# Kernel tuning notes

Measured on AMD Instinct MI355X. Metric: run time of the kernel, lower is better.

Reference implementation:

```python
import jax, jax.numpy as jnp
import numpy as np
from jax import lax

# ---- config (mirrors cfg.* used by the module) ----
ANCHOR_RATIOS = (0.5, 1.0, 2.0)
ANCHOR_SCALES = (8.0, 16.0, 32.0)
FEATURE_STRIDE = 16
BASE_SIZE = 40  # generate_anchors(40, ...)
BN_EPS = 1e-5
LOG_CLAMP = 1e-30  # torch uses 1e-300, which underflows to 0 in fp32; use fp32-safe tiny


def generate_anchors(base_size=BASE_SIZE, ratios=ANCHOR_RATIOS, scales=ANCHOR_SCALES):
    """py-faster-rcnn style anchor generation, corner format (x1,y1,x2,y2). -> (A,4)"""
    w = h = float(base_size)
    cx = (base_size - 1) * 0.5
    cy = (base_size - 1) * 0.5
    size = w * h
    out = []
    for r in ratios:
        ws = np.round(np.sqrt(size / r))
        hs = np.round(ws * r)
        for s in scales:
            W, H = ws * s, hs * s
            out.append([cx - 0.5 * (W - 1), cy - 0.5 * (H - 1),
                        cx + 0.5 * (W - 1), cy + 0.5 * (H - 1)])
    return np.asarray(out, dtype=np.float32)  # (A,4)


def splash_anchors(fH, fW, n, base_anchors, stride):
    """Shift base anchors over the feature grid. -> (n, fH*fW*A, 4), row-major H,W then A."""
    sx = jnp.arange(fW, dtype=jnp.float32) * stride
    sy = jnp.arange(fH, dtype=jnp.float32) * stride
    SY, SX = jnp.meshgrid(sy, sx, indexing='ij')            # (fH,fW)
    shifts = jnp.stack([SX, SY, SX, SY], axis=-1).reshape(-1, 1, 4)  # (fH*fW,1,4)
    anc = (shifts + jnp.asarray(base_anchors)[None, :, :]).reshape(-1, 4)  # (fH*fW*A,4)
    return jnp.broadcast_to(anc[None], (n, anc.shape[0], 4))


def conv2d(x, w, b, pad):
    y = lax.conv_general_dilated(x, w, (1, 1), [(pad, pad), (pad, pad)],
                                 dimension_numbers=('NCHW', 'OIHW', 'NCHW'))
    return y + b[None, :, None, None]


def batchnorm_train(x, gamma, beta):
    # training-mode BN: per-channel batch stats over (N,H,W), biased variance
    m = jnp.mean(x, axis=(0, 2, 3), keepdims=True)
    v = jnp.mean(jnp.square(x - m), axis=(0, 2, 3), keepdims=True)
    xn = (x - m) * lax.rsqrt(v + BN_EPS)
    return xn * gamma[None, :, None, None] + beta[None, :, None, None]


def mish(x):
    return x * jnp.tanh(jax.nn.softplus(x))


def corner2center(b):
    w = b[..., 2] - b[..., 0]
    h = b[..., 3] - b[..., 1]
    cx = b[..., 0] + 0.5 * w
    cy = b[..., 1] + 0.5 * h
    return jnp.stack([cx, cy, w, h], axis=-1)


def setup_inputs() -> dict:
    key = jax.random.key(0)
    ks = jax.random.split(key, 7)
    C_IN, C_BASE, A = 256, 256, 9
    x = jax.random.normal(ks[0], (8, C_IN, 128, 128), dtype=jnp.float32)
    # kaiming-uniform-ish scaled weights
    def kaiming(k, shape):
        fan_in = shape[1] * shape[2] * shape[3]
        bound = float(np.sqrt(6.0 / fan_in))
        return jax.random.uniform(k, shape, jnp.float32, -bound, bound)
    return {
        "x": x,
        "W_base": kaiming(ks[1], (C_BASE, C_IN, 3, 3)),
        "b_base": jnp.zeros((C_BASE,), jnp.float32),
        "g_base": jnp.ones((C_BASE,), jnp.float32),
        "be_base": jnp.zeros((C_BASE,), jnp.float32),
        "W_cls": kaiming(ks[2], (2 * A, C_BASE, 1, 1)),
        "b_cls": jnp.zeros((2 * A,), jnp.float32),
        "g_cls": jnp.ones((2 * A,), jnp.float32),
        "be_cls": jnp.zeros((2 * A,), jnp.float32),
        "W_reg": kaiming(ks[3], (4 * A, C_BASE, 1, 1)),
        "b_reg": jnp.zeros((4 * A,), jnp.float32),
        "g_reg": jnp.ones((4 * A,), jnp.float32),
        "be_reg": jnp.zeros((4 * A,), jnp.float32),
        "img_size": 2048,
    }


def reference(x, W_base, b_base, g_base, be_base,
              W_cls, b_cls, g_cls, be_cls,
              W_reg, b_reg, g_reg, be_reg, img_size):
    n, c, fH, fW = x.shape
    A = 9
    # BASE_CONV: Conv3x3 -> Mish -> Dropout2d (identity here, deterministic) -> BN
    base = batchnorm_train(mish(conv2d(x, W_base, b_base, 1)), g_base, be_base)

    anchors = splash_anchors(fH, fW, n, generate_anchors(), FEATURE_STRIDE)  # (n,K,4) corners

    rpn_reg = batchnorm_train(conv2d(base, W_reg, b_reg, 0), g_reg, be_reg)
    rpn_reg = jnp.transpose(rpn_reg, (0, 2, 3, 1)).reshape(n, -1, 4)          # (n,K,4)

    rpn_score = batchnorm_train(conv2d(base, W_cls, b_cls, 0), g_cls, be_cls)
    rpn_score = jnp.transpose(rpn_score, (0, 2, 3, 1)).reshape(n, fH, fW, A, 2)
    fg_scores = jax.nn.softmax(rpn_score, axis=4)[..., 1].reshape(n, -1)      # (n,K)

    rpn_reg = rpn_reg + anchors                                               # decoded corners

    # proposal layer: clip proposals to the image, keep all (fixed-shape)
    lim = jnp.float32(img_size)
    rois = jnp.clip(rpn_reg, 0.0, lim)                                        # (n,K,4) corners
    rois = corner2center(rois)                                                # (cx,cy,w,h)

    anc_c = corner2center(anchors)
    tx = (rois[..., 0] - anc_c[..., 0]) / anc_c[..., 2]
    ty = (rois[..., 1] - anc_c[..., 1]) / anc_c[..., 3]
    tw = jnp.log(jnp.maximum(rois[..., 2] / anc_c[..., 2], LOG_CLAMP))
    th = jnp.log(jnp.maximum(rois[..., 3] / anc_c[..., 3], LOG_CLAMP))
    ts = jnp.stack([tx, ty, tw, th], axis=-1)
    return (fg_scores, ts, rois)
```

## Files before the change

### kernel.cpp

```cpp
#include <hip/hip_runtime.h>
#include <stdint.h>

typedef short bf16x8 __attribute__((ext_vector_type(8)));
typedef float f32x4 __attribute__((ext_vector_type(4)));

#define AS1 __attribute__((address_space(1)))
#define AS3 __attribute__((address_space(3)))

static __device__ __forceinline__ void gl16(const void* g, void* l) {
  __builtin_amdgcn_global_load_lds((const AS1 void*)g, (AS3 void*)l, 16, 0, 0);
}

static __device__ __forceinline__ unsigned short f2bf(float f) {
  unsigned u = __float_as_uint(f);
  u = u + 0x7fffu + ((u >> 16) & 1u);
  return (unsigned short)(u >> 16);
}
static __device__ __forceinline__ float bf2f(unsigned short h) {
  return __uint_as_float(((unsigned)h) << 16);
}
static __device__ __forceinline__ float mishf(float x) {
  float sp = fmaxf(x, 0.f) + log1pf(expf(-fabsf(x)));
  float e2 = expf(-2.f * sp);
  float th = (1.f - e2) / (1.f + e2);
  return x * th;
}

#define NIMG 8
#define HH 128
#define WW 128
#define HP 130
#define CIN 256
#define MPIX (NIMG * HH * WW)
#define KTOT 2304
#define FGCNT (MPIX * 9)
#define TSCNT (MPIX * 9 * 4)

__device__ __constant__ float AW[9] = {456.f, 912.f, 1824.f, 320.f, 640.f, 1280.f, 224.f, 448.f, 896.f};
__device__ __constant__ float AH[9] = {224.f, 448.f, 896.f, 320.f, 640.f, 1280.f, 448.f, 896.f, 1792.f};

__global__ __launch_bounds__(256) void k_wt(const float* __restrict__ Wb,
                                            unsigned short* __restrict__ Wt2) {
  int d = blockIdx.x * 256 + threadIdx.x;
  int c = d & 31, oc = (d >> 5) & 255, s = d >> 13;
  int kh = s / 24, r = s % 24, kw = r >> 3, icb = r & 7;
  int ic = icb * 32 + c;
  Wt2[d] = f2bf(Wb[((oc * 256 + ic) * 3 + kh) * 3 + kw]);
}

__global__ __launch_bounds__(256) void k_tr(const float* __restrict__ x,
                                            unsigned short* __restrict__ xt2) {
  __shared__ float tile[32][129];
  int b = blockIdx.x;
  int icb = b & 7, h = (b >> 3) & 127, n = b >> 10;
  int t = threadIdx.x;
  const float* src = x + (((size_t)(n * 256 + icb * 32) * 128 + h) * 128);
#pragma unroll
  for (int i = 0; i < 4; ++i) {
    int idx = t + 256 * i;
    int w4 = idx & 31, ic = idx >> 5;
    float4 v = *(const float4*)(src + (size_t)ic * 16384 + w4 * 4);
    tile[ic][w4 * 4 + 0] = v.x; tile[ic][w4 * 4 + 1] = v.y;
    tile[ic][w4 * 4 + 2] = v.z; tile[ic][w4 * 4 + 3] = v.w;
  }
  __syncthreads();
#pragma unroll
  for (int i = 0; i < 8; ++i) {
    int idx = t + 256 * i;
    int icp = idx & 15, w = idx >> 4;
    unsigned lo = f2bf(tile[icp * 2][w]);
    unsigned hi = f2bf(tile[icp * 2 + 1][w]);
    size_t pix = ((size_t)(icb * 8 + n) * HP + (h + 1)) * HP + (w + 1);
    *(unsigned*)(xt2 + pix * 32 + icp * 2) = lo | (hi << 16);
  }
}

__global__ __launch_bounds__(256) void k_bord(unsigned short* __restrict__ xt2) {
  int tid = blockIdx.x * 256 + threadIdx.x;
  int chunk = tid & 3, pix = tid >> 2;
  int nn = pix / 516, bp = pix % 516;
  int hp, wp;
  if (bp < 130) { hp = 0; wp = bp; }
  else if (bp < 260) { hp = 129; wp = bp - 130; }
  else { int r = bp - 260; hp = 1 + (r >> 1); wp = (r & 1) ? 129 : 0; }
  size_t off = (((size_t)nn * HP + hp) * HP + wp) * 32 + chunk * 8;
  uint4 z = {0u, 0u, 0u, 0u};
  *(uint4*)(xt2 + off) = z;
}

__global__ __launch_bounds__(256) void k_conv(const unsigned short* __restrict__ xt2,
                                              const unsigned short* __restrict__ Wt2,
                                              const float* __restrict__ b_base,
                                              unsigned short* __restrict__ yt2,
                                              float* __restrict__ statsA) {
  __shared__ __align__(16) char lds[16384];
  int t = threadIdx.x;
  int lane = t & 63, w4 = t >> 6;
  int wr = w4 >> 1, wc = w4 & 1;
  int row16 = lane & 15, kgl = lane >> 4;
  int pr = lane & 15, pq = lane >> 4;

  int bid = blockIdx.x;
  int swz = (bid & 7) * 256 + (bid >> 3);
  int pixb = swz >> 1, oh = swz & 1;
  int n = pixb >> 7, h0 = pixb & 127;
  size_t M0 = (size_t)pixb * 128;

  f32x4 acc[4][4];
#pragma unroll
  for (int m = 0; m < 4; ++m)
#pragma unroll
    for (int nf = 0; nf < 4; ++nf) { f32x4 z = {0.f, 0.f, 0.f, 0.f}; acc[m][nf] = z; }

  const unsigned short* aS0 =
      xt2 + ((size_t)(n * HP + h0) * HP + w4 * 32 + pr) * 32 + pq * 8;
  const unsigned short* aS1 = aS0 + 16 * 32;
  const unsigned short* bS0 = Wt2 + (size_t)(oh * 128 + w4 * 32 + pr) * 32 + pq * 8;
  const unsigned short* bS1 = bS0 + 16 * 32;
  char* dA0 = lds + (2 * w4) * 1024;
  char* dA1 = lds + (2 * w4 + 1) * 1024;
  char* dB0 = lds + 8192 + (2 * w4) * 1024;
  char* dB1 = lds + 8192 + (2 * w4 + 1) * 1024;

  int aoffA = wr * 4096 + kgl * 256 + row16 * 16;
  int aoffB = wc * 4096 + kgl * 256 + row16 * 16;
  const size_t planeStride = (size_t)8 * HP * HP * 32;

  int s = 0;
  for (int kh = 0; kh < 3; ++kh) {
    for (int kw = 0; kw < 3; ++kw) {
      for (int icb = 0; icb < 8; ++icb, ++s) {
        size_t offA = (size_t)icb * planeStride + ((size_t)kh * HP + kw) * 32;
        size_t offB = (size_t)s * 8192;
        gl16(aS0 + offA, dA0);
        gl16(aS1 + offA, dA1);
        gl16(bS0 + offB, dB0);
        gl16(bS1 + offB, dB1);
        __syncthreads();
        bf16x8 af[4], bfr[4];
#pragma unroll
        for (int m = 0; m < 4; ++m) af[m] = *(const bf16x8*)(lds + aoffA + m * 1024);
#pragma unroll
        for (int nf = 0; nf < 4; ++nf) bfr[nf] = *(const bf16x8*)(lds + 8192 + aoffB + nf * 1024);
#pragma unroll
        for (int m = 0; m < 4; ++m)
#pragma unroll
          for (int nf = 0; nf < 4; ++nf)
            acc[m][nf] = __builtin_amdgcn_mfma_f32_16x16x32_bf16(af[m], bfr[nf], acc[m][nf], 0, 0, 0);
        __syncthreads();
      }
    }
  }

  float sums[4] = {0.f, 0.f, 0.f, 0.f}, sumq[4] = {0.f, 0.f, 0.f, 0.f};
#pragma unroll
  for (int nf = 0; nf < 4; ++nf) {
    int oc = oh * 128 + wc * 64 + nf * 16 + row16;
    float bias = b_base[oc];
    size_t obase = (size_t)(oc >> 5) * MPIX * 32 + (oc & 31);
#pragma unroll
    for (int m = 0; m < 4; ++m) {
#pragma unroll
      for (int j = 0; j < 4; ++j) {
        int p = wr * 64 + m * 16 + kgl * 4 + j;
        float y = mishf(acc[m][nf][j] + bias);
        yt2[obase + (M0 + p) * 32] = f2bf(y);
        sums[nf] += y; sumq[nf] += y * y;
      }
    }
  }
#pragma unroll
  for (int nf = 0; nf < 4; ++nf) {
    float s1 = sums[nf], s2 = sumq[nf];
    s1 += __shfl_xor(s1, 16); s2 += __shfl_xor(s2, 16);
    s1 += __shfl_xor(s1, 32); s2 += __shfl_xor(s2, 32);
    if (lane < 16) {
      int oc = oh * 128 + wc * 64 + nf * 16 + lane;
      atomicAdd(&statsA[oc], s1);
      atomicAdd(&statsA[256 + oc], s2);
    }
  }
}

__global__ __launch_bounds__(256) void k_fold(const float* __restrict__ statsA,
                                              const float* __restrict__ g_base,
                                              const float* __restrict__ be_base,
                                              const float* __restrict__ W_cls,
                                              const float* __restrict__ b_cls,
                                              const float* __restrict__ W_reg,
                                              const float* __restrict__ b_reg,
                                              unsigned short* __restrict__ W2t2,
                                              float* __restrict__ b2) {
  __shared__ float sS[256], sT[256];
  int t = threadIdx.x;
  {
    float cnt = (float)MPIX;
    float m = statsA[t] / cnt;
    float v = fmaxf(statsA[256 + t] / cnt - m * m, 0.f);
    float s = g_base[t] * rsqrtf(v + 1e-5f);
    sS[t] = s;
    sT[t] = be_base[t] - m * s;
  }
  __syncthreads();
  if (t < 64) {
    float bias = 0.f;
    if (t < 36) bias = b_reg[t];
    else if (t < 54) bias = b_cls[t - 36];
    float acc = 0.f;
    for (int ic = 0; ic < 256; ++ic) {
      float w = 0.f;
      if (t < 36) w = W_reg[t * 256 + ic];
      else if (t < 54) w = W_cls[(t - 36) * 256 + ic];
      acc += w * sT[ic];
      W2t2[((size_t)(ic >> 5) * 64 + t) * 32 + (ic & 31)] = f2bf(w * sS[ic]);
    }
    b2[t] = bias + acc;
  }
}

__global__ __launch_bounds__(256) void k_mm2(const unsigned short* __restrict__ yt2,
                                             const unsigned short* __restrict__ W2t2,
                                             const float* __restrict__ b2,
                                             unsigned short* __restrict__ zt,
                                             float* __restrict__ statsZ) {
  __shared__ __align__(16) char lds2[12288];
  int t = threadIdx.x, lane = t & 63, w4 = t >> 6;
  int row16 = lane & 15, kgl = lane >> 4;
  int pr = lane & 15, pq = lane >> 4;
  size_t pixbase = (size_t)blockIdx.x * 128;

  f32x4 acc[2][4];
#pragma unroll
  for (int m = 0; m < 2; ++m)
#pragma unroll
    for (int nn = 0; nn < 4; ++nn) { f32x4 z = {0.f, 0.f, 0.f, 0.f}; acc[m][nn] = z; }

  const unsigned short* aS0 = yt2 + (pixbase + w4 * 32 + pr) * 32 + pq * 8;
  const unsigned short* aS1 = aS0 + 16 * 32;
  const unsigned short* bS = W2t2 + (size_t)(w4 * 16 + pr) * 32 + pq * 8;
  char* dA0 = lds2 + (2 * w4) * 1024;
  char* dA1 = lds2 + (2 * w4 + 1) * 1024;
  char* dB  = lds2 + 8192 + w4 * 1024;

  int aoffA = w4 * 2048 + kgl * 256 + row16 * 16;
  int aoffB = kgl * 256 + row16 * 16;

  for (int s = 0; s < 8; ++s) {
    size_t ao = (size_t)s * MPIX * 32;
    size_t bo = (size_t)s * 2048;
    gl16(aS0 + ao, dA0);
    gl16(aS1 + ao, dA1);
    gl16(bS + bo, dB);
    __syncthreads();
    bf16x8 af[2], bfr[4];
#pragma unroll
    for (int m = 0; m < 2; ++m) af[m] = *(const bf16x8*)(lds2 + aoffA + m * 1024);
#pragma unroll
    for (int nn = 0; nn < 4; ++nn) bfr[nn] = *(const bf16x8*)(lds2 + 8192 + aoffB + nn * 1024);
#pragma unroll
    for (int m = 0; m < 2; ++m)
#pragma unroll
      for (int nn = 0; nn < 4; ++nn)
        acc[m][nn] = __builtin_amdgcn_mfma_f32_16x16x32_bf16(af[m], bfr[nn], acc[m][nn], 0, 0, 0);
    __syncthreads();
  }

  float sums[4] = {0.f, 0.f, 0.f, 0.f}, sumq[4] = {0.f, 0.f, 0.f, 0.f};
#pragma unroll
  for (int nn = 0; nn < 4; ++nn) {
    int oc = nn * 16 + row16;
    float bias = b2[oc];
#pragma unroll
    for (int m = 0; m < 2; ++m) {
#pragma unroll
      for (int j = 0; j < 4; ++j) {
        int p = w4 * 32 + m * 16 + kgl * 4 + j;
        float v = acc[m][nn][j] + bias;
        zt[(pixbase + p) * 64 + oc] = f2bf(v);
        sums[nn] += v; sumq[nn] += v * v;
      }
    }
  }
#pragma unroll
  for (int nn = 0; nn < 4; ++nn) {
    float s1 = sums[nn], s2 = sumq[nn];
    s1 += __shfl_xor(s1, 16); s2 += __shfl_xor(s2, 16);
    s1 += __shfl_xor(s1, 32); s2 += __shfl_xor(s2, 32);
    if (lane < 16) {
      int oc = nn * 16 + lane;
      atomicAdd(&statsZ[oc], s1);
      atomicAdd(&statsZ[64 + oc], s2);
    }
  }
}

__global__ __launch_bounds__(64) void k_zstat(const float* __restrict__ statsZ,
                                              const float* __restrict__ g_cls,
                                              const float* __restrict__ be_cls,
                                              const float* __restrict__ g_reg,
                                              const float* __restrict__ be_reg,
                                              float* __restrict__ zsc,
                                              float* __restrict__ zsh) {
  int t = threadIdx.x;
  float g = 1.f, be = 0.f;
  if (t < 36) { g = g_reg[t]; be = be_reg[t]; }
  else if (t < 54) { g = g_cls[t - 36]; be = be_cls[t - 36]; }
  float cnt = (float)MPIX;
  float m = statsZ[t] / cnt;
  float v = fmaxf(statsZ[64 + t] / cnt - m * m, 0.f);
  float s = g * rsqrtf(v + 1e-5f);
  zsc[t] = s;
  zsh[t] = be - m * s;
}

__global__ __launch_bounds__(256) void k_dec(const unsigned short* __restrict__ zt,
                                             const float* __restrict__ zsc,
                                             const float* __restrict__ zsh,
                                             const int* __restrict__ imgsz,
                                             float* __restrict__ out) {
  int p = blockIdx.x * 256 + threadIdx.x;
  float lim = (float)imgsz[0];
  float zn[64];
  {
    const uint4* zp4 = (const uint4*)(zt + (size_t)p * 64);
#pragma unroll
    for (int i = 0; i < 8; ++i) {
      uint4 v = zp4[i];
      unsigned a0 = v.x, a1 = v.y, a2 = v.z, a3 = v.w;
      zn[i * 8 + 0] = bf2f((unsigned short)(a0 & 0xffff));
      zn[i * 8 + 1] = bf2f((unsigned short)(a0 >> 16));
      zn[i * 8 + 2] = bf2f((unsigned short)(a1 & 0xffff));
      zn[i * 8 + 3] = bf2f((unsigned short)(a1 >> 16));
      zn[i * 8 + 4] = bf2f((unsigned short)(a2 & 0xffff));
      zn[i * 8 + 5] = bf2f((unsigned short)(a2 >> 16));
      zn[i * 8 + 6] = bf2f((unsigned short)(a3 & 0xffff));
      zn[i * 8 + 7] = bf2f((unsigned short)(a3 >> 16));
    }
#pragma unroll
    for (int i = 0; i < 54; ++i) zn[i] = zn[i] * zsc[i] + zsh[i];
  }
  int rem = p & 16383, h = rem >> 7, w = rem & 127;
  float fx = 16.f * (float)w, fy = 16.f * (float)h;
  size_t kbase = (size_t)p * 9;
  float* fgout = out;
  float* tsout = out + FGCNT;
  float* roout = out + FGCNT + TSCNT;
#pragma unroll
  for (int a = 0; a < 9; ++a) {
    float x1 = 20.f - 0.5f * AW[a] + fx;
    float y1 = 20.f - 0.5f * AH[a] + fy;
    float x2 = 19.f + 0.5f * AW[a] + fx;
    float y2 = 19.f + 0.5f * AH[a] + fy;
    float cx1 = fminf(fmaxf(x1 + zn[4 * a + 0], 0.f), lim);
    float cy1 = fminf(fmaxf(y1 + zn[4 * a + 1], 0.f), lim);
    float cx2 = fminf(fmaxf(x2 + zn[4 * a + 2], 0.f), lim);
    float cy2 = fminf(fmaxf(y2 + zn[4 * a + 3], 0.f), lim);
    float bw = cx2 - cx1, bh = cy2 - cy1;
    float cx = cx1 + 0.5f * bw, cy = cy1 + 0.5f * bh;
    float aw = AW[a] - 1.f, ah = AH[a] - 1.f;
    float acx = 19.5f + fx, acy = 19.5f + fy;
    float tx = (cx - acx) / aw, ty = (cy - acy) / ah;
    float tw = logf(fmaxf(bw / aw, 1e-30f));
    float th = logf(fmaxf(bh / ah, 1e-30f));
    float s0 = zn[36 + 2 * a], s1 = zn[36 + 2 * a + 1];
    float fg = 1.f / (1.f + expf(s0 - s1));
    fgout[kbase + a] = fg;
    size_t o4 = (kbase + a) * 4;
    tsout[o4 + 0] = tx; tsout[o4 + 1] = ty; tsout[o4 + 2] = tw; tsout[o4 + 3] = th;
    roout[o4 + 0] = cx; roout[o4 + 1] = cy; roout[o4 + 2] = bw; roout[o4 + 3] = bh;
  }
}

extern "C" void kernel_launch(void* const* d_in, const int* in_sizes, int n_in,
                              void* d_out, int out_size, void* d_ws, size_t ws_size,
                              hipStream_t stream) {
  const float* x   = (const float*)d_in[0];
  const float* Wb  = (const float*)d_in[1];
  const float* bb  = (const float*)d_in[2];
  const float* gb  = (const float*)d_in[3];
  const float* beb = (const float*)d_in[4];
  const float* Wc  = (const float*)d_in[5];
  const float* bc  = (const float*)d_in[6];
  const float* gc  = (const float*)d_in[7];
  const float* bec = (const float*)d_in[8];
  const float* Wr  = (const float*)d_in[9];
  const float* br  = (const float*)d_in[10];
  const float* gr  = (const float*)d_in[11];
  const float* ber = (const float*)d_in[12];
  const int* imgsz = (const int*)d_in[13];

  char* ws = (char*)d_ws;
  const size_t OFF_XTP = 0;
  const size_t OFF_Y   = 69222400;
  const size_t OFF_Z   = 136331264;
  const size_t OFF_WT  = 153108480;
  const size_t OFF_W2  = 154288128;
  const size_t OFF_S   = 154320896;
  unsigned short* xt2  = (unsigned short*)(ws + OFF_XTP);
  unsigned short* yt2  = (unsigned short*)(ws + OFF_Y);
  unsigned short* zt   = (unsigned short*)(ws + OFF_Z);
  unsigned short* Wt2  = (unsigned short*)(ws + OFF_WT);
  unsigned short* W2t2 = (unsigned short*)(ws + OFF_W2);
  float* b2     = (float*)(ws + OFF_S);
  float* statsA = (float*)(ws + OFF_S + 256);
  float* statsZ = (float*)(ws + OFF_S + 2304);
  float* zsc    = (float*)(ws + OFF_S + 2816);
  float* zsh    = (float*)(ws + OFF_S + 3072);
  float* out = (float*)d_out;

  hipMemsetAsync(statsA, 0, (512 + 128) * sizeof(float), stream);
  k_wt  <<<2304, 256, 0, stream>>>(Wb, Wt2);
  k_tr  <<<8192, 256, 0, stream>>>(x, xt2);
  k_bord<<<516, 256, 0, stream>>>(xt2);
  k_conv<<<2048, 256, 0, stream>>>(xt2, Wt2, bb, yt2, statsA);
  k_fold<<<1, 256, 0, stream>>>(statsA, gb, beb, Wc, bc, Wr, br, W2t2, b2);
  k_mm2 <<<1024, 256, 0, stream>>>(yt2, W2t2, b2, zt, statsZ);
  k_zstat<<<1, 64, 0, stream>>>(statsZ, gc, bec, gr, ber, zsc, zsh);
  k_dec <<<512, 256, 0, stream>>>(zt, zsc, zsh, imgsz, out);
}
```

Baseline: 546.5 us.

## Double-buffer LDS stages in conv and 1x1 matmul kernels

Both MFMA kernels (the 3x3 conv and the 1x1 second matmul) now keep two LDS buffers. The global-to-LDS load for the next K-slice is issued right after a single barrier and then overlaps the MFMA work on the current slice, replacing the old load, sync, compute, sync pattern. This doubles LDS use per block, which could reduce occupancy. Whether real overlap happens depends on the compiler not inserting conservative vmcnt waits before the LDS reads.

```diff
diff --git a/kernel.cpp b/kernel.cpp
--- a/kernel.cpp
+++ b/kernel.cpp
@@ -93,7 +93,7 @@
                                               const float* __restrict__ b_base,
                                               unsigned short* __restrict__ yt2,
                                               float* __restrict__ statsA) {
-  __shared__ __align__(16) char lds[16384];
+  __shared__ __align__(16) char lds[32768];
   int t = threadIdx.x;
   int lane = t & 63, w4 = t >> 6;
   int wr = w4 >> 1, wc = w4 & 1;
@@ -117,39 +117,43 @@
   const unsigned short* aS1 = aS0 + 16 * 32;
   const unsigned short* bS0 = Wt2 + (size_t)(oh * 128 + w4 * 32 + pr) * 32 + pq * 8;
   const unsigned short* bS1 = bS0 + 16 * 32;
-  char* dA0 = lds + (2 * w4) * 1024;
-  char* dA1 = lds + (2 * w4 + 1) * 1024;
-  char* dB0 = lds + 8192 + (2 * w4) * 1024;
-  char* dB1 = lds + 8192 + (2 * w4 + 1) * 1024;
-
+
+  const size_t planeStride = (size_t)8 * HP * HP * 32;
   int aoffA = wr * 4096 + kgl * 256 + row16 * 16;
   int aoffB = wc * 4096 + kgl * 256 + row16 * 16;
-  const size_t planeStride = (size_t)8 * HP * HP * 32;
-
-  int s = 0;
-  for (int kh = 0; kh < 3; ++kh) {
-    for (int kw = 0; kw < 3; ++kw) {
-      for (int icb = 0; icb < 8; ++icb, ++s) {
-        size_t offA = (size_t)icb * planeStride + ((size_t)kh * HP + kw) * 32;
-        size_t offB = (size_t)s * 8192;
-        gl16(aS0 + offA, dA0);
-        gl16(aS1 + offA, dA1);
-        gl16(bS0 + offB, dB0);
-        gl16(bS1 + offB, dB1);
-        __syncthreads();
-        bf16x8 af[4], bfr[4];
-#pragma unroll
-        for (int m = 0; m < 4; ++m) af[m] = *(const bf16x8*)(lds + aoffA + m * 1024);
-#pragma unroll
-        for (int nf = 0; nf < 4; ++nf) bfr[nf] = *(const bf16x8*)(lds + 8192 + aoffB + nf * 1024);
-#pragma unroll
-        for (int m = 0; m < 4; ++m)
-#pragma unroll
-          for (int nf = 0; nf < 4; ++nf)
-            acc[m][nf] = __builtin_amdgcn_mfma_f32_16x16x32_bf16(af[m], bfr[nf], acc[m][nf], 0, 0, 0);
-        __syncthreads();
-      }
-    }
+
+  auto STAGE = [&](int sv, int c_) {
+    int icb_ = sv & 7;
+    int khw = sv >> 3;
+    int kh_ = khw / 3;
+    int kw_ = khw - kh_ * 3;
+    size_t offA = (size_t)icb_ * planeStride + ((size_t)kh_ * HP + kw_) * 32;
+    size_t offB = (size_t)sv * 8192;
+    char* buf = lds + c_ * 16384;
+    gl16(aS0 + offA, buf + (2 * w4) * 1024);
+    gl16(aS1 + offA, buf + (2 * w4 + 1) * 1024);
+    gl16(bS0 + offB, buf + 8192 + (2 * w4) * 1024);
+    gl16(bS1 + offB, buf + 8192 + (2 * w4 + 1) * 1024);
+  };
+
+  STAGE(0, 0);
+  int cur = 0;
+  for (int s = 0; s < 72; ++s) {
+    __syncthreads();
+    if (s < 71) STAGE(s + 1, cur ^ 1);
+    const char* ab = lds + cur * 16384;
+    const char* bb = ab + 8192;
+    bf16x8 af[4], bfr[4];
+#pragma unroll
+    for (int m = 0; m < 4; ++m) af[m] = *(const bf16x8*)(ab + aoffA + m * 1024);
+#pragma unroll
+    for (int nf = 0; nf < 4; ++nf) bfr[nf] = *(const bf16x8*)(bb + aoffB + nf * 1024);
+#pragma unroll
+    for (int m = 0; m < 4; ++m)
+#pragma unroll
+      for (int nf = 0; nf < 4; ++nf)
+        acc[m][nf] = __builtin_amdgcn_mfma_f32_16x16x32_bf16(af[m], bfr[nf], acc[m][nf], 0, 0, 0);
+    cur ^= 1;
   }
 
   float sums[4] = {0.f, 0.f, 0.f, 0.f}, sumq[4] = {0.f, 0.f, 0.f, 0.f};
@@ -223,7 +227,7 @@
                                              const float* __restrict__ b2,
                                              unsigned short* __restrict__ zt,
                                              float* __restrict__ statsZ) {
-  __shared__ __align__(16) char lds2[12288];
+  __shared__ __align__(16) char lds2[24576];
   int t = threadIdx.x, lane = t & 63, w4 = t >> 6;
   int row16 = lane & 15, kgl = lane >> 4;
   int pr = lane & 15, pq = lane >> 4;
@@ -238,31 +242,37 @@
   const unsigned short* aS0 = yt2 + (pixbase + w4 * 32 + pr) * 32 + pq * 8;
   const unsigned short* aS1 = aS0 + 16 * 32;
   const unsigned short* bS = W2t2 + (size_t)(w4 * 16 + pr) * 32 + pq * 8;
-  char* dA0 = lds2 + (2 * w4) * 1024;
-  char* dA1 = lds2 + (2 * w4 + 1) * 1024;
-  char* dB  = lds2 + 8192 + w4 * 1024;
 
   int aoffA = w4 * 2048 + kgl * 256 + row16 * 16;
   int aoffB = kgl * 256 + row16 * 16;
 
-  for (int s = 0; s < 8; ++s) {
+  auto STG = [&](int s, int c_) {
     size_t ao = (size_t)s * MPIX * 32;
     size_t bo = (size_t)s * 2048;
-    gl16(aS0 + ao, dA0);
-    gl16(aS1 + ao, dA1);
-    gl16(bS + bo, dB);
+    char* buf = lds2 + c_ * 12288;
+    gl16(aS0 + ao, buf + (2 * w4) * 1024);
+    gl16(aS1 + ao, buf + (2 * w4 + 1) * 1024);
+    gl16(bS + bo, buf + 8192 + w4 * 1024);
+  };
+
+  STG(0, 0);
+  int cur = 0;
+  for (int s = 0; s < 8; ++s) {
     __syncthreads();
+    if (s < 7) STG(s + 1, cur ^ 1);
+    const char* ab = lds2 + cur * 12288;
+    const char* bb = ab + 8192;
     bf16x8 af[2], bfr[4];
 #pragma unroll
-    for (int m = 0; m < 2; ++m) af[m] = *(const bf16x8*)(lds2 + aoffA + m * 1024);
-#pragma unroll
-    for (int nn = 0; nn < 4; ++nn) bfr[nn] = *(const bf16x8*)(lds2 + 8192 + aoffB + nn * 1024);
+    for (int m = 0; m < 2; ++m) af[m] = *(const bf16x8*)(ab + aoffA + m * 1024);
+#pragma unroll
+    for (int nn = 0; nn < 4; ++nn) bfr[nn] = *(const bf16x8*)(bb + aoffB + nn * 1024);
 #pragma unroll
     for (int m = 0; m < 2; ++m)
 #pragma unroll
       for (int nn = 0; nn < 4; ++nn)
         acc[m][nn] = __builtin_amdgcn_mfma_f32_16x16x32_bf16(af[m], bfr[nn], acc[m][nn], 0, 0, 0);
-    __syncthreads();
+    cur ^= 1;
   }
 
   float sums[4] = {0.f, 0.f, 0.f, 0.f}, sumq[4] = {0.f, 0.f, 0.f, 0.f};
```

After: 536.1 us. About the same (-1.9%).
